# Kernel tuning notes

Hardware: AMD Instinct MI355X
Metric: run time of the kernel (lower is better)

## Reference

```python
import jax, jax.numpy as jnp
import numpy as np

NUM_GRAPHS = 2048  # number of graphs in the batch (max batch id + 1)


def setup_inputs() -> dict:
    key = jax.random.key(0)
    ks = jax.random.split(key, 8)
    N, E, ND, ED, H = 100000, 400000, 256, 128, 128
    IN = ND * 3 + ED  # 896
    h = jax.random.normal(ks[0], (N, ND), dtype=jnp.float32)
    ei = jax.random.randint(ks[1], (2, E), 0, N, dtype=jnp.int64)
    ea = jax.random.normal(ks[2], (E, ED), dtype=jnp.float32)
    batch = jnp.sort(jax.random.randint(ks[3], (N,), 0, NUM_GRAPHS, dtype=jnp.int64))
    W1 = jax.random.normal(ks[4], (IN, H), dtype=jnp.float32) * (1.0 / np.sqrt(IN))
    b1 = jnp.zeros((H,), dtype=jnp.float32)
    W2 = jax.random.normal(ks[5], (H, 1), dtype=jnp.float32) * (1.0 / np.sqrt(H))
    b2 = jnp.zeros((1,), dtype=jnp.float32)
    return {"h": h, "ei": ei, "ea": ea, "batch": batch,
            "W1": W1, "b1": b1, "W2": W2, "b2": b2}


def reference(h, ei, ea, batch, W1, b1, W2, b2):
    s, t = ei[0], ei[1]
    # global_mean_pool: per-graph mean of node features
    sums = jax.ops.segment_sum(h, batch, num_segments=NUM_GRAPHS)          # [B, ND]
    counts = jax.ops.segment_sum(jnp.ones((h.shape[0],), h.dtype), batch,
                                 num_segments=NUM_GRAPHS)                   # [B]
    pooled = sums / jnp.maximum(counts, 1.0)[:, None]
    g = pooled[batch[s]]                                                    # [E, ND]
    x = jnp.concatenate([h[s], h[t], ea, g], axis=-1)                       # [E, 3*ND+ED]
    hid = jnp.maximum(x @ W1 + b1, 0.0)
    return hid @ W2 + b2                                                    # [E, 1]
```

## Files before the change

kernel.cpp:

```cpp
#include <hip/hip_runtime.h>
#include <hip/hip_bf16.h>


typedef __attribute__((ext_vector_type(8))) short bf16x8;
typedef __attribute__((ext_vector_type(4))) float f32x4;

constexpr int kND = 256;
constexpr int kED = 128;
constexpr int kH  = 128;
constexpr int kIN = 896;
constexpr int kKT = 7;
constexpr int kB  = 2048;
constexpr int TM  = 128;
constexpr int kNF = 224;

__device__ __forceinline__ ushort f2bf(float x) {
  union { float f; unsigned u; } c; c.f = x;
  unsigned u = c.u + 0x7FFFu + ((c.u >> 16) & 1u);
  return (ushort)(u >> 16);
}
__device__ __forceinline__ float bf2f(ushort x) {
  union { unsigned u; float f; } c; c.u = ((unsigned)x) << 16;
  return c.f;
}
__device__ __forceinline__ bool data_is_f32(const void* p) {
  const unsigned* u = (const unsigned*)p;
  int cnt = 0;
  #pragma unroll
  for (int i = 0; i < 64; ++i) {
    unsigned e = (u[i] >> 7) & 0xFFu;
    cnt += (e >= 90u && e <= 140u) ? 1 : 0;
  }
  return cnt < 40;
}
__device__ __forceinline__ bool idx_is_64(const int* __restrict__ p) {
  return ((p[1] | p[3] | p[5] | p[7]) == 0) && ((p[0] | p[2] | p[4] | p[6]) != 0);
}
__device__ __forceinline__ float loadf(const void* p, int i, bool isf32) {
  return isf32 ? ((const float*)p)[i] : bf2f(((const ushort*)p)[i]);
}
__device__ __forceinline__ bf16x8 cvt8(const float* p) {
  float4 f0 = ((const float4*)p)[0];
  float4 f1 = ((const float4*)p)[1];
  union { ushort us[8]; bf16x8 v; } cv;
  cv.us[0] = f2bf(f0.x); cv.us[1] = f2bf(f0.y);
  cv.us[2] = f2bf(f0.z); cv.us[3] = f2bf(f0.w);
  cv.us[4] = f2bf(f1.x); cv.us[5] = f2bf(f1.y);
  cv.us[6] = f2bf(f1.z); cv.us[7] = f2bf(f1.w);
  return cv.v;
}

__global__ __launch_bounds__(256) void pool_kernel(
    const void* __restrict__ hv, ushort* __restrict__ hbf, int preconv,
    const int* __restrict__ batch, const int* __restrict__ ei, int N,
    ushort* __restrict__ pooled) {
  const bool isf32 = data_is_f32(hv);
  const bool is64 = idx_is_64(ei);
  const int b = blockIdx.x, tid = threadIdx.x;
  __shared__ int bounds[2];
  __shared__ float sred[8][kND];
  if (tid < 2) {
    int target = b + tid;
    int lo = 0, hi = N;
    while (lo < hi) {
      int mid = (lo + hi) >> 1;
      int v = is64 ? batch[2 * mid] : batch[mid];
      if (v < target) lo = mid + 1; else hi = mid;
    }
    bounds[tid] = lo;
  }
  __syncthreads();
  const int lo = bounds[0], hi = bounds[1];
  const int dg = tid & 31;
  const int rstr = tid >> 5;
  float a[8];
  #pragma unroll
  for (int j = 0; j < 8; ++j) a[j] = 0.f;

  if (!isf32) {
    const ushort* base = (const ushort*)hv + dg * 8;
    int r = lo + rstr;
    for (; r + 8 < hi; r += 16) {
      union { uint4 v; ushort us[8]; } u0, u1;
      u0.v = *(const uint4*)(base + (size_t)r * kND);
      u1.v = *(const uint4*)(base + (size_t)(r + 8) * kND);
      #pragma unroll
      for (int j = 0; j < 8; ++j) a[j] += bf2f(u0.us[j]);
      #pragma unroll
      for (int j = 0; j < 8; ++j) a[j] += bf2f(u1.us[j]);
    }
    for (; r < hi; r += 8) {
      union { uint4 v; ushort us[8]; } u0;
      u0.v = *(const uint4*)(base + (size_t)r * kND);
      #pragma unroll
      for (int j = 0; j < 8; ++j) a[j] += bf2f(u0.us[j]);
    }
  } else if (preconv) {
    const float* base = (const float*)hv + dg * 8;
    ushort* wb = hbf + dg * 8;
    for (int r = lo + rstr; r < hi; r += 8) {
      float4 f0 = *(const float4*)(base + (size_t)r * kND);
      float4 f1 = *(const float4*)(base + (size_t)r * kND + 4);
      union { ushort us[8]; uint4 v; } cv;
      cv.us[0] = f2bf(f0.x); cv.us[1] = f2bf(f0.y);
      cv.us[2] = f2bf(f0.z); cv.us[3] = f2bf(f0.w);
      cv.us[4] = f2bf(f1.x); cv.us[5] = f2bf(f1.y);
      cv.us[6] = f2bf(f1.z); cv.us[7] = f2bf(f1.w);
      *(uint4*)(wb + (size_t)r * kND) = cv.v;
      a[0] += f0.x; a[1] += f0.y; a[2] += f0.z; a[3] += f0.w;
      a[4] += f1.x; a[5] += f1.y; a[6] += f1.z; a[7] += f1.w;
    }
  } else {
    const float* base = (const float*)hv + dg * 8;
    for (int r = lo + rstr; r < hi; r += 8) {
      float4 f0 = *(const float4*)(base + (size_t)r * kND);
      float4 f1 = *(const float4*)(base + (size_t)r * kND + 4);
      a[0] += f0.x; a[1] += f0.y; a[2] += f0.z; a[3] += f0.w;
      a[4] += f1.x; a[5] += f1.y; a[6] += f1.z; a[7] += f1.w;
    }
  }
  #pragma unroll
  for (int j = 0; j < 8; ++j) sred[rstr][dg * 8 + j] = a[j];
  __syncthreads();
  int cnt = hi - lo; if (cnt < 1) cnt = 1;
  float inv = 1.f / (float)cnt;
  float s = 0.f;
  #pragma unroll
  for (int st = 0; st < 8; ++st) s += sred[st][tid];
  pooled[(size_t)b * kND + tid] = f2bf(s * inv);
}

__global__ __launch_bounds__(256) void build_wfrag(
    const void* __restrict__ W1v, ushort* __restrict__ Wfrag) {
  const bool isf32 = data_is_f32(W1v);
  int idx = blockIdx.x * 256 + threadIdx.x;
  if (idx >= kNF * 64) return;
  int l = idx & 63, f = idx >> 6;
  int ni = f & 3, nhi = (f >> 2) & 1, ksg = f >> 3;
  int tile = ksg >> 2;
  int basek = (tile == 0) ? 512 : ((tile < 5) ? (tile - 1) * 128 : tile * 128);
  int n = nhi * 64 + ni * 16 + (l & 15);
  int k0 = basek + (ksg & 3) * 32 + (l >> 4) * 8;
  union { ushort us[8]; uint4 v; } cv;
  #pragma unroll
  for (int j = 0; j < 8; ++j)
    cv.us[j] = f2bf(loadf(W1v, (k0 + j) * kH + n, isf32));
  *(uint4*)(Wfrag + (size_t)f * 512 + l * 8) = cv.v;
}

__global__ __launch_bounds__(256, 3) void edge_kernel(
    const void* __restrict__ hv, const ushort* __restrict__ hbf, int preconv,
    const int* __restrict__ ei, const void* __restrict__ eav,
    const int* __restrict__ batch, const ushort* __restrict__ pooled,
    const ushort* __restrict__ Wfrag, const void* __restrict__ b1v,
    const void* __restrict__ W2v, const void* __restrict__ b2v,
    void* __restrict__ outv, int E) {
  __shared__ int rs[TM], rt[TM], rg[TM];
  __shared__ float outacc[TM];
  __shared__ float b1s[kH], w2s[kH];

  const int tid = threadIdx.x;
  const int e0 = blockIdx.x * TM;
  const bool isf32 = data_is_f32(hv);
  const bool is64 = idx_is_64(ei);

  if (tid < TM) {
    int e = e0 + tid; if (e >= E) e = E - 1;
    int s = is64 ? ei[2 * e] : ei[e];
    int t = is64 ? ei[2 * (E + e)] : ei[E + e];
    rs[tid] = s;
    rt[tid] = t;
    rg[tid] = is64 ? batch[2 * s] : batch[s];
    w2s[tid] = loadf(W2v, tid, isf32);
    b1s[tid] = loadf(b1v, tid, isf32);
    outacc[tid] = 0.f;
  }
  __syncthreads();

  const int wave = tid >> 6, lane = tid & 63;
  const int l15 = lane & 15, quad = lane >> 4;
  const int mh = (wave & 1) * 64;
  const int nhi = wave >> 1;
  const int nh = nhi * 64;

  const ushort* hp = isf32 ? (preconv ? hbf : nullptr) : (const ushort*)hv;
  const bool hb = (hp != nullptr);
  const bool ea32 = data_is_f32(eav);

  const char* bS[4]; const char* bT[4]; const ushort* bG[4]; const char* bE[4];
  #pragma unroll
  for (int mi = 0; mi < 4; ++mi) {
    int r = mh + mi * 16 + l15;
    int e = e0 + r; if (e >= E) e = E - 1;
    if (hb) {
      bS[mi] = (const char*)(hp + (size_t)rs[r] * kND + quad * 8);
      bT[mi] = (const char*)(hp + (size_t)rt[r] * kND + quad * 8);
    } else {
      bS[mi] = (const char*)((const float*)hv + (size_t)rs[r] * kND + quad * 8);
      bT[mi] = (const char*)((const float*)hv + (size_t)rt[r] * kND + quad * 8);
    }
    bG[mi] = pooled + (size_t)rg[r] * kND + quad * 8;
    bE[mi] = ea32 ? (const char*)((const float*)eav + (size_t)e * kED + quad * 8)
                  : (const char*)((const ushort*)eav + (size_t)e * kED + quad * 8);
  }

  f32x4 acc[4][4];
  #pragma unroll
  for (int i = 0; i < 4; ++i)
    #pragma unroll
    for (int j = 0; j < 4; ++j)
      acc[i][j] = (f32x4){0.f, 0.f, 0.f, 0.f};

  const ushort* wl = Wfrag + (size_t)nhi * 2048 + lane * 8;

  #pragma unroll
  for (int kt = 0; kt < kKT; ++kt) {
    #pragma unroll
    for (int ks = 0; ks < 4; ++ks) {
      const int ksg = kt * 4 + ks;
      bf16x8 bfm[4];
      #pragma unroll
      for (int ni = 0; ni < 4; ++ni)
        bfm[ni] = *(const bf16x8*)(wl + (size_t)ksg * 4096 + ni * 512);
      bf16x8 af[4];
      #pragma unroll
      for (int mi = 0; mi < 4; ++mi) {
        if (kt == 0) {
          af[mi] = ea32 ? cvt8((const float*)bE[mi] + ks * 32)
                        : *(const bf16x8*)((const ushort*)bE[mi] + ks * 32);
        } else if (kt < 3) {
          af[mi] = hb ? *(const bf16x8*)(bS[mi] + (kt - 1) * 256 + ks * 64)
                      : cvt8((const float*)(bS[mi] + (size_t)(kt - 1) * 512 + ks * 128));
        } else if (kt < 5) {
          af[mi] = hb ? *(const bf16x8*)(bT[mi] + (kt - 3) * 256 + ks * 64)
                      : cvt8((const float*)(bT[mi] + (size_t)(kt - 3) * 512 + ks * 128));
        } else {
          af[mi] = *(const bf16x8*)(bG[mi] + (kt - 5) * 128 + ks * 32);
        }
      }
      #pragma unroll
      for (int mi = 0; mi < 4; ++mi)
        #pragma unroll
        for (int ni = 0; ni < 4; ++ni)
          acc[mi][ni] = __builtin_amdgcn_mfma_f32_16x16x32_bf16(
              af[mi], bfm[ni], acc[mi][ni], 0, 0, 0);
    }
  }

  float w2v[4], b1r[4];
  #pragma unroll
  for (int ni = 0; ni < 4; ++ni) {
    int n = nh + ni * 16 + l15;
    w2v[ni] = w2s[n];
    b1r[ni] = b1s[n];
  }
  #pragma unroll
  for (int mi = 0; mi < 4; ++mi) {
    float ps[4] = {0.f, 0.f, 0.f, 0.f};
    #pragma unroll
    for (int ni = 0; ni < 4; ++ni)
      #pragma unroll
      for (int j = 0; j < 4; ++j) {
        float v = acc[mi][ni][j] + b1r[ni];
        ps[j] += (v > 0.f ? v : 0.f) * w2v[ni];
      }
    #pragma unroll
    for (int off = 1; off < 16; off <<= 1)
      #pragma unroll
      for (int j = 0; j < 4; ++j)
        ps[j] += __shfl_xor(ps[j], off, 64);
    if (l15 == 0)
      #pragma unroll
      for (int j = 0; j < 4; ++j)
        atomicAdd(&outacc[mh + mi * 16 + quad * 4 + j], ps[j]);
  }
  __syncthreads();
  if (tid < TM) {
    int e = e0 + tid;
    if (e < E) {
      float a = outacc[tid] + loadf(b2v, 0, isf32);
      if (isf32) ((float*)outv)[e] = a;
      else       ((ushort*)outv)[e] = f2bf(a);
    }
  }
}

extern "C" void kernel_launch(void* const* d_in, const int* in_sizes, int n_in,
                              void* d_out, int out_size, void* d_ws, size_t ws_size,
                              hipStream_t stream) {
  const void* h   = d_in[0];
  const int*  ei  = (const int*)d_in[1];
  const void* ea  = d_in[2];
  const int*  bat = (const int*)d_in[3];
  const void* W1  = d_in[4];
  const void* b1  = d_in[5];
  const void* W2  = d_in[6];
  const void* b2  = d_in[7];

  const int N = in_sizes[3];
  const int E = in_sizes[1] / 2;

  ushort* pooled = (ushort*)d_ws;
  ushort* Wfrag  = pooled + (size_t)kB * kND;
  ushort* hbf    = Wfrag + (size_t)kNF * 512;
  const size_t need =
      ((size_t)kB * kND + (size_t)kNF * 512 + (size_t)N * kND) * sizeof(ushort);
  const int preconv = (ws_size >= need) ? 1 : 0;

  pool_kernel<<<kB, 256, 0, stream>>>(h, hbf, preconv, bat, ei, N, pooled);
  build_wfrag<<<(kNF * 64 + 255) / 256, 256, 0, stream>>>(W1, Wfrag);
  edge_kernel<<<(E + TM - 1) / TM, 256, 0, stream>>>(
      h, hbf, preconv, ei, ea, bat, pooled, Wfrag, b1, W2, b2, d_out, E);
}
```

Before: 573.8 us.

## Stage gathered edge rows into LDS via async global_load_lds with double buffering

The edge kernel now gathers the concatenated input rows (edge attrs, source/target node features, pooled graph features) into a double-buffered, XOR-swizzled LDS tile using global_load_lds, prefetching the next K chunk while MFMAs consume the current one. Before this, each wave loaded its A fragments straight from global memory with scattered 16-byte reads. Data-type variants are dispatched through compile-time templates. The 64KB of LDS lowers the occupancy hint from 3 to 2 blocks per CU and adds a barrier per chunk.

```diff
diff --git a/kernel.cpp b/kernel.cpp
--- a/kernel.cpp
+++ b/kernel.cpp
@@ -4,15 +4,21 @@
 
 typedef __attribute__((ext_vector_type(8))) short bf16x8;
 typedef __attribute__((ext_vector_type(4))) float f32x4;
+typedef __attribute__((address_space(3))) char lds_char;
+typedef __attribute__((address_space(1))) const void g_cvoid;
 
 constexpr int kND = 256;
 constexpr int kED = 128;
 constexpr int kH  = 128;
-constexpr int kIN = 896;
-constexpr int kKT = 7;
 constexpr int kB  = 2048;
 constexpr int TM  = 128;
 constexpr int kNF = 224;
+
+__device__ __forceinline__ void gl2lds16(const void* gsrc, lds_char* ldst) {
+  __builtin_amdgcn_global_load_lds((g_cvoid*)gsrc,
+                                   (__attribute__((address_space(3))) void*)ldst,
+                                   16, 0, 0);
+}
 
 __device__ __forceinline__ ushort f2bf(float x) {
   union { float f; unsigned u; } c; c.f = x;
@@ -38,16 +44,6 @@
 }
 __device__ __forceinline__ float loadf(const void* p, int i, bool isf32) {
   return isf32 ? ((const float*)p)[i] : bf2f(((const ushort*)p)[i]);
-}
-__device__ __forceinline__ bf16x8 cvt8(const float* p) {
-  float4 f0 = ((const float4*)p)[0];
-  float4 f1 = ((const float4*)p)[1];
-  union { ushort us[8]; bf16x8 v; } cv;
-  cv.us[0] = f2bf(f0.x); cv.us[1] = f2bf(f0.y);
-  cv.us[2] = f2bf(f0.z); cv.us[3] = f2bf(f0.w);
-  cv.us[4] = f2bf(f1.x); cv.us[5] = f2bf(f1.y);
-  cv.us[6] = f2bf(f1.z); cv.us[7] = f2bf(f1.w);
-  return cv.v;
 }
 
 __global__ __launch_bounds__(256) void pool_kernel(
@@ -148,16 +144,136 @@
   *(uint4*)(Wfrag + (size_t)f * 512 + l * 8) = cv.v;
 }
 
-__global__ __launch_bounds__(256, 3) void edge_kernel(
+template<bool HB, bool EA32> struct TD;
+template<> struct TD<true, true> {
+  static constexpr int NT = 8;
+  static constexpr int ty[8]  = {0,0,1,1,2,2,3,3};
+  static constexpr int sub[8] = {0,1,0,1,0,1,0,1};
+  static constexpr int ksc[8] = {2,2,4,4,4,4,4,4};
+  static constexpr int kg0[8] = {0,2,4,8,12,16,20,24};
+  static constexpr bool tf32[8] = {1,1,0,0,0,0,0,0};
+};
+template<> struct TD<true, false> {
+  static constexpr int NT = 7;
+  static constexpr int ty[7]  = {0,1,1,2,2,3,3};
+  static constexpr int sub[7] = {0,0,1,0,1,0,1};
+  static constexpr int ksc[7] = {4,4,4,4,4,4,4};
+  static constexpr int kg0[7] = {0,4,8,12,16,20,24};
+  static constexpr bool tf32[7] = {0,0,0,0,0,0,0};
+};
+template<> struct TD<false, true> {
+  static constexpr int NT = 12;
+  static constexpr int ty[12]  = {0,0,1,1,1,1,2,2,2,2,3,3};
+  static constexpr int sub[12] = {0,1,0,1,2,3,0,1,2,3,0,1};
+  static constexpr int ksc[12] = {2,2,2,2,2,2,2,2,2,2,4,4};
+  static constexpr int kg0[12] = {0,2,4,6,8,10,12,14,16,18,20,24};
+  static constexpr bool tf32[12] = {1,1,1,1,1,1,1,1,1,1,0,0};
+};
+template<> struct TD<false, false> {
+  static constexpr int NT = 11;
+  static constexpr int ty[11]  = {0,1,1,1,1,2,2,2,2,3,3};
+  static constexpr int sub[11] = {0,0,1,2,3,0,1,2,3,0,1};
+  static constexpr int ksc[11] = {4,2,2,2,2,2,2,2,2,4,4};
+  static constexpr int kg0[11] = {0,4,6,8,10,12,14,16,18,20,24};
+  static constexpr bool tf32[11] = {0,1,1,1,1,1,1,1,1,0,0};
+};
+
+template<bool HB, bool EA32>
+__device__ __forceinline__ void edge_core(
+    const char* __restrict__ hsrc, const char* __restrict__ easrc,
+    const ushort* __restrict__ pooled, const ushort* __restrict__ Wfrag,
+    const char* XlB, lds_char* Xl3, const int* rs, const int* rt, const int* rg,
+    int e0, int E, int wave, int lane, f32x4 (&acc)[4][4]) {
+  using T = TD<HB, EA32>;
+  const int l15 = lane & 15, quad = lane >> 4;
+  const int mh = (wave & 1) * 64;
+  const int nhi = wave >> 1;
+  const ushort* wl = Wfrag + (size_t)nhi * 2048 + lane * 8;
+  const int cx0 = (lane & 15) * 16;
+  const int rlane = lane >> 4;
+
+  auto src_addr = [&](int t, int row) -> const char* {
+    int cx = cx0 ^ ((row & 7) << 4);
+    int ty = T::ty[t], sub = T::sub[t];
+    if (ty == 0) {
+      int e = e0 + row; if (e >= E) e = E - 1;
+      return easrc + (size_t)e * (EA32 ? 512 : 256) + sub * 256 + cx;
+    }
+    if (ty == 1) return hsrc + (size_t)rs[row] * (HB ? 512 : 1024) + sub * 256 + cx;
+    if (ty == 2) return hsrc + (size_t)rt[row] * (HB ? 512 : 1024) + sub * 256 + cx;
+    return (const char*)pooled + (size_t)rg[row] * 512 + sub * 256 + cx;
+  };
+  auto stage = [&](int t) {
+    lds_char* dst = Xl3 + (t & 1) * 32768;
+    #pragma unroll
+    for (int i = 0; i < 8; ++i) {
+      int row = wave * 32 + i * 4 + rlane;
+      gl2lds16(src_addr(t, row), dst + (wave * 32 + i * 4) * 256);
+    }
+  };
+
+  stage(0);
+  __syncthreads();
+
+  #pragma unroll
+  for (int t = 0; t < T::NT; ++t) {
+    bf16x8 bq[16];
+    #pragma unroll
+    for (int ks = 0; ks < T::ksc[t]; ++ks)
+      #pragma unroll
+      for (int ni = 0; ni < 4; ++ni)
+        bq[ks * 4 + ni] =
+            *(const bf16x8*)(wl + (size_t)(T::kg0[t] + ks) * 4096 + ni * 512);
+    __builtin_amdgcn_sched_barrier(0);
+    if (t + 1 < T::NT) stage(t + 1);
+
+    const char* xb = XlB + (t & 1) * 32768;
+    #pragma unroll
+    for (int ks = 0; ks < T::ksc[t]; ++ks) {
+      bf16x8 af[4];
+      #pragma unroll
+      for (int mi = 0; mi < 4; ++mi) {
+        int row = mh + mi * 16 + l15;
+        int sz = (row & 7) << 4;
+        const char* rb = xb + row * 256;
+        if (T::tf32[t]) {
+          int cb = ks * 128 + quad * 32;
+          float4 f0 = *(const float4*)(rb + (cb ^ sz));
+          float4 f1 = *(const float4*)(rb + ((cb + 16) ^ sz));
+          union { ushort us[8]; bf16x8 v; } cv;
+          cv.us[0] = f2bf(f0.x); cv.us[1] = f2bf(f0.y);
+          cv.us[2] = f2bf(f0.z); cv.us[3] = f2bf(f0.w);
+          cv.us[4] = f2bf(f1.x); cv.us[5] = f2bf(f1.y);
+          cv.us[6] = f2bf(f1.z); cv.us[7] = f2bf(f1.w);
+          af[mi] = cv.v;
+        } else {
+          int cb = ks * 64 + quad * 16;
+          af[mi] = *(const bf16x8*)(rb + (cb ^ sz));
+        }
+      }
+      #pragma unroll
+      for (int mi = 0; mi < 4; ++mi)
+        #pragma unroll
+        for (int ni = 0; ni < 4; ++ni)
+          acc[mi][ni] = __builtin_amdgcn_mfma_f32_16x16x32_bf16(
+              af[mi], bq[ks * 4 + ni], acc[mi][ni], 0, 0, 0);
+    }
+    __syncthreads();
+  }
+}
+
+__global__ __launch_bounds__(256, 2) void edge_kernel(
     const void* __restrict__ hv, const ushort* __restrict__ hbf, int preconv,
     const int* __restrict__ ei, const void* __restrict__ eav,
     const int* __restrict__ batch, const ushort* __restrict__ pooled,
     const ushort* __restrict__ Wfrag, const void* __restrict__ b1v,
     const void* __restrict__ W2v, const void* __restrict__ b2v,
     void* __restrict__ outv, int E) {
+  __shared__ __align__(16) char XlB[2 * 32768];
   __shared__ int rs[TM], rt[TM], rg[TM];
   __shared__ float outacc[TM];
   __shared__ float b1s[kH], w2s[kH];
+  lds_char* Xl3 = (lds_char*)XlB;
 
   const int tid = threadIdx.x;
   const int e0 = blockIdx.x * TM;
@@ -183,27 +299,6 @@
   const int nhi = wave >> 1;
   const int nh = nhi * 64;
 
-  const ushort* hp = isf32 ? (preconv ? hbf : nullptr) : (const ushort*)hv;
-  const bool hb = (hp != nullptr);
-  const bool ea32 = data_is_f32(eav);
-
-  const char* bS[4]; const char* bT[4]; const ushort* bG[4]; const char* bE[4];
-  #pragma unroll
-  for (int mi = 0; mi < 4; ++mi) {
-    int r = mh + mi * 16 + l15;
-    int e = e0 + r; if (e >= E) e = E - 1;
-    if (hb) {
-      bS[mi] = (const char*)(hp + (size_t)rs[r] * kND + quad * 8);
-      bT[mi] = (const char*)(hp + (size_t)rt[r] * kND + quad * 8);
-    } else {
-      bS[mi] = (const char*)((const float*)hv + (size_t)rs[r] * kND + quad * 8);
-      bT[mi] = (const char*)((const float*)hv + (size_t)rt[r] * kND + quad * 8);
-    }
-    bG[mi] = pooled + (size_t)rg[r] * kND + quad * 8;
-    bE[mi] = ea32 ? (const char*)((const float*)eav + (size_t)e * kED + quad * 8)
-                  : (const char*)((const ushort*)eav + (size_t)e * kED + quad * 8);
-  }
-
   f32x4 acc[4][4];
   #pragma unroll
   for (int i = 0; i < 4; ++i)
@@ -211,40 +306,21 @@
     for (int j = 0; j < 4; ++j)
       acc[i][j] = (f32x4){0.f, 0.f, 0.f, 0.f};
 
-  const ushort* wl = Wfrag + (size_t)nhi * 2048 + lane * 8;
-
-  #pragma unroll
-  for (int kt = 0; kt < kKT; ++kt) {
-    #pragma unroll
-    for (int ks = 0; ks < 4; ++ks) {
-      const int ksg = kt * 4 + ks;
-      bf16x8 bfm[4];
-      #pragma unroll
-      for (int ni = 0; ni < 4; ++ni)
-        bfm[ni] = *(const bf16x8*)(wl + (size_t)ksg * 4096 + ni * 512);
-      bf16x8 af[4];
-      #pragma unroll
-      for (int mi = 0; mi < 4; ++mi) {
-        if (kt == 0) {
-          af[mi] = ea32 ? cvt8((const float*)bE[mi] + ks * 32)
-                        : *(const bf16x8*)((const ushort*)bE[mi] + ks * 32);
-        } else if (kt < 3) {
-          af[mi] = hb ? *(const bf16x8*)(bS[mi] + (kt - 1) * 256 + ks * 64)
-                      : cvt8((const float*)(bS[mi] + (size_t)(kt - 1) * 512 + ks * 128));
-        } else if (kt < 5) {
-          af[mi] = hb ? *(const bf16x8*)(bT[mi] + (kt - 3) * 256 + ks * 64)
-                      : cvt8((const float*)(bT[mi] + (size_t)(kt - 3) * 512 + ks * 128));
-        } else {
-          af[mi] = *(const bf16x8*)(bG[mi] + (kt - 5) * 128 + ks * 32);
-        }
-      }
-      #pragma unroll
-      for (int mi = 0; mi < 4; ++mi)
-        #pragma unroll
-        for (int ni = 0; ni < 4; ++ni)
-          acc[mi][ni] = __builtin_amdgcn_mfma_f32_16x16x32_bf16(
-              af[mi], bfm[ni], acc[mi][ni], 0, 0, 0);
-    }
+  const bool hb = !isf32 || preconv;
+  const char* hsrc = !isf32 ? (const char*)hv
+                            : (preconv ? (const char*)hbf : (const char*)hv);
+  const bool ea32 = data_is_f32(eav);
+
+  if (hb) {
+    if (ea32) edge_core<true, true >((const char*)hsrc, (const char*)eav, pooled,
+                                     Wfrag, XlB, Xl3, rs, rt, rg, e0, E, wave, lane, acc);
+    else      edge_core<true, false>((const char*)hsrc, (const char*)eav, pooled,
+                                     Wfrag, XlB, Xl3, rs, rt, rg, e0, E, wave, lane, acc);
+  } else {
+    if (ea32) edge_core<false, true >((const char*)hsrc, (const char*)eav, pooled,
+                                      Wfrag, XlB, Xl3, rs, rt, rg, e0, E, wave, lane, acc);
+    else      edge_core<false, false>((const char*)hsrc, (const char*)eav, pooled,
+                                      Wfrag, XlB, Xl3, rs, rt, rg, e0, E, wave, lane, acc);
   }
 
   float w2v[4], b1r[4];
```

Result: faster. 499.4 us (-13.0%).
